# Performance work log

Measured on AMD Instinct MI355X. Metric: run time of the kernel, lower is better.

The kernel has to match this reference:

```python
import jax, jax.numpy as jnp
import numpy as np

N_NODES = 50000
N_EDGES = 1_600_000
IN_DIM = 128
HID = 32
HEADS = 4
NEG_SLOPE = 0.2


def setup_inputs() -> dict:
    key = jax.random.key(0)
    ks = jax.random.split(key, 6)
    h = jax.random.normal(ks[0], (N_NODES, IN_DIM), dtype=jnp.float32)
    src = jax.random.randint(ks[1], (N_EDGES,), 0, N_NODES, dtype=jnp.int32)
    dst = jax.random.randint(ks[2], (N_EDGES,), 0, N_NODES, dtype=jnp.int32)
    s = 1.0 / np.sqrt(IN_DIM)  # ~ Linear default init scale
    Wq = (jax.random.normal(ks[3], (HEADS, IN_DIM, HID), dtype=jnp.float32) * s)
    Wk = (jax.random.normal(ks[4], (HEADS, IN_DIM, HID), dtype=jnp.float32) * s)
    Wv = (jax.random.normal(ks[5], (HEADS, IN_DIM, HID), dtype=jnp.float32) * s)
    return {"h": h, "src": src, "dst": dst, "Wq": Wq, "Wk": Wk, "Wv": Wv}


def _gat_forward(h, src, dst, Wq, Wk, Wv):
    n = h.shape[0]
    # per-head projections: [H, N, D]
    q = jnp.einsum('ni,hio->hno', h, Wq)
    k = jnp.einsum('ni,hio->hno', h, Wk)
    v = jnp.einsum('ni,hio->hno', h, Wv)
    # edge scores: e = leaky_relu(<q_src, k_dst>)  -> [H, E]
    e = jax.nn.leaky_relu(jnp.einsum('hed,hed->he', q[:, src], k[:, dst]),
                          negative_slope=NEG_SLOPE)
    # segment softmax over incoming edges of each dst node
    seg_max = jax.vmap(lambda x: jax.ops.segment_max(x, dst, num_segments=n))(e)
    seg_max = jax.lax.stop_gradient(jnp.where(jnp.isfinite(seg_max), seg_max, 0.0))
    ex = jnp.exp(e - seg_max[:, dst])                       # [H, E]
    denom = jax.vmap(lambda x: jax.ops.segment_sum(x, dst, num_segments=n))(ex)
    alpha = ex / jnp.maximum(denom, 1e-9)[:, dst]           # [H, E]
    # weighted scatter-sum of source values into dst nodes: [H, N, D]
    msg = alpha[..., None] * v[:, src]
    out = jax.vmap(lambda m: jax.ops.segment_sum(m, dst, num_segments=n))(msg)
    # concat heads along feature dim -> [N, H*D]
    return out.transpose(1, 0, 2).reshape(n, HEADS * HID)


def reference(h, src, dst, Wq, Wk, Wv):
    return _gat_forward(h, src, dst, Wq, Wk, Wv)
```

## Files before the change

kernel.cpp:

```cpp
#include <hip/hip_runtime.h>
#include <hip/hip_fp16.h>

#define IN_DIM 128
#define HID 32
#define HEADS 4
#define OUTC (HEADS*HID)
#define NEG_SLOPE 0.2f
#define BSH 4
#define BN 16
#define BCAP 768
#define NBMAX 3200
#define NCOLS 384
#define WPB 192

typedef _Float16 f16x8 __attribute__((ext_vector_type(8)));
typedef float    f32x4 __attribute__((ext_vector_type(4)));

__device__ __forceinline__ unsigned short f2h(float f) {
    return __half_as_ushort(__float2half_rn(f));
}
__device__ __forceinline__ float2 h2f2(unsigned u) {
    __half2 h = *reinterpret_cast<__half2*>(&u);
    return __half22float2(h);
}
__device__ __forceinline__ float qdot(const uint4& qv, const float4& kd) {
    float2 a = h2f2(qv.x);
    float2 b = h2f2(qv.y);
    return a.x * kd.x + a.y * kd.y + b.x * kd.z + b.y * kd.w;
}
__device__ __forceinline__ void vacc(const uint4& qv, float e, float4& acc) {
    float2 a = h2f2(qv.z);
    float2 b = h2f2(qv.w);
    acc.x = fmaf(e, a.x, acc.x);
    acc.y = fmaf(e, a.y, acc.y);
    acc.z = fmaf(e, b.x, acc.z);
    acc.w = fmaf(e, b.y, acc.w);
}

__global__ __launch_bounds__(256) void prep_bin(
    const float* __restrict__ Wq, const float* __restrict__ Wk,
    const float* __restrict__ Wv, unsigned short* __restrict__ Wt,
    const int* __restrict__ src, const int* __restrict__ dst,
    int* __restrict__ gcount, unsigned* __restrict__ pairs,
    int ne, int nbuck)
{
    const int tid = threadIdx.x;

    if (blockIdx.x < WPB) {
        int idx = blockIdx.x * 256 + tid;
        if (idx < NCOLS * IN_DIM) {
            int c = idx >> 7, k = idx & 127;
            int sel = c >> 7;
            int cc  = c & 127;
            int head = cc >> 5, dcol = cc & 31;
            const float* W = (sel == 0) ? Wk : (sel == 1) ? Wq : Wv;
            Wt[idx] = f2h(W[(size_t)head * IN_DIM * HID + (size_t)k * HID + dcol]);
        }
        return;
    }

    __shared__ int hist[NBMAX];
    __shared__ int base[NBMAX];
    const int bblk = blockIdx.x - WPB;

    for (int i = tid; i < nbuck; i += 256) hist[i] = 0;
    __syncthreads();

    const int ne4 = ne >> 2;
    const int4* s4 = (const int4*)src;
    const int4* d4 = (const int4*)dst;

    int4 sv[4], dv[4];
    int loc[16], bk[16];
    bool val[4];
#pragma unroll
    for (int k = 0; k < 4; ++k) {
        int idx = bblk * 1024 + k * 256 + tid;
        val[k] = idx < ne4;
        if (val[k]) { sv[k] = s4[idx]; dv[k] = d4[idx]; }
        else { sv[k] = make_int4(0,0,0,0); dv[k] = make_int4(0,0,0,0); }
    }
#pragma unroll
    for (int k = 0; k < 4; ++k) {
        int dd[4] = { dv[k].x, dv[k].y, dv[k].z, dv[k].w };
#pragma unroll
        for (int j = 0; j < 4; ++j) {
            int b = dd[j] >> BSH;
            bk[k*4+j]  = b;
            loc[k*4+j] = val[k] ? atomicAdd(&hist[b], 1) : 0;
        }
    }
    __syncthreads();
    for (int i = tid; i < nbuck; i += 256)
        base[i] = hist[i] ? atomicAdd(&gcount[i], hist[i]) : 0;
    __syncthreads();
#pragma unroll
    for (int k = 0; k < 4; ++k) {
        if (!val[k]) continue;
        int ss[4] = { sv[k].x, sv[k].y, sv[k].z, sv[k].w };
        int dd[4] = { dv[k].x, dv[k].y, dv[k].z, dv[k].w };
#pragma unroll
        for (int j = 0; j < 4; ++j) {
            int b = bk[k*4+j];
            int p = base[b] + loc[k*4+j];
            if (p < BCAP)
                pairs[(size_t)b * BCAP + p] =
                    ((unsigned)ss[j] << BSH) | (unsigned)(dd[j] & (BN-1));
        }
    }
    if (bblk == 0 && tid == 0) {
        for (int e = ne4 * 4; e < ne; ++e) {
            int b = dst[e] >> BSH;
            int p = atomicAdd(&gcount[b], 1);
            if (p < BCAP)
                pairs[(size_t)b * BCAP + p] =
                    ((unsigned)src[e] << BSH) | (unsigned)(dst[e] & (BN-1));
        }
    }
}

__global__ __launch_bounds__(256) void gat_proj_mfma(
    const float* __restrict__ h, const unsigned short* __restrict__ Wt,
    unsigned short* __restrict__ Ko, unsigned short* __restrict__ QV, int n)
{
    __shared__ unsigned short hsm[32 * IN_DIM];
    const int tid  = threadIdx.x;
    const int row0 = blockIdx.x * 32;

    for (int idx = tid; idx < 32 * 64; idx += 256) {
        int r  = idx >> 6;
        int c2 = idx & 63;
        int gr = row0 + r;
        float2 hv = (gr < n) ? ((const float2*)h)[(size_t)gr * 64 + c2]
                             : make_float2(0.f, 0.f);
        int col = c2 * 2;
        int sc  = col ^ ((r & 7) << 3);
        __half2 packed = __floats2half2_rn(hv.x, hv.y);
        *(unsigned*)&hsm[r * IN_DIM + sc] = *(unsigned*)&packed;
    }
    __syncthreads();

    const int w = tid >> 6;
    const int l = tid & 63;
    const int l15 = l & 15;
    const int kg  = l >> 4;
    const _Float16* Wt16 = (const _Float16*)Wt;

    f32x4 acc[2][6];
#pragma unroll
    for (int rt = 0; rt < 2; ++rt)
#pragma unroll
        for (int ct = 0; ct < 6; ++ct) acc[rt][ct] = (f32x4){0.f, 0.f, 0.f, 0.f};

#pragma unroll
    for (int s = 0; s < 4; ++s) {
        int scol = (s * 32 + kg * 8) ^ ((l & 7) << 3);
        f16x8 a0 = *(const f16x8*)&hsm[l15 * IN_DIM + scol];
        f16x8 a1 = *(const f16x8*)&hsm[(l15 + 16) * IN_DIM + scol];
#pragma unroll
        for (int ct = 0; ct < 6; ++ct) {
            int c = w * 96 + ct * 16 + l15;
            f16x8 b = *(const f16x8*)&Wt16[(size_t)c * IN_DIM + s * 32 + kg * 8];
            acc[0][ct] = __builtin_amdgcn_mfma_f32_16x16x32_f16(a0, b, acc[0][ct], 0, 0, 0);
            acc[1][ct] = __builtin_amdgcn_mfma_f32_16x16x32_f16(a1, b, acc[1][ct], 0, 0, 0);
        }
    }

#pragma unroll
    for (int rt = 0; rt < 2; ++rt) {
#pragma unroll
        for (int ct = 0; ct < 6; ++ct) {
            int cD = w * 96 + ct * 16 + l15;
#pragma unroll
            for (int r = 0; r < 4; ++r) {
                int node = row0 + rt * 16 + kg * 4 + r;
                if (node >= n) continue;
                float v = acc[rt][ct][r];
                if (cD < 128) {
                    Ko[(size_t)node * OUTC + cD] = f2h(v);
                } else if (cD < 256) {
                    int cq = cD - 128;
                    QV[(size_t)node * 256 + (cq >> 2) * 8 + (cq & 3)] = f2h(v);
                } else {
                    int cv = cD - 256;
                    QV[(size_t)node * 256 + (cv >> 2) * 8 + (cv & 3) + 4] = f2h(v);
                }
            }
        }
    }
}

__global__ __launch_bounds__(256) void gat_bucket(
    const unsigned* __restrict__ pairs, const int* __restrict__ gcount,
    const uint4* __restrict__ QV, const ushort4* __restrict__ K2,
    float* __restrict__ out, int n, int nbuck)
{
    __shared__ unsigned short sl[BCAP];
    __shared__ int cl[BN], cur[BN], off[BN + 1];

    const int b   = blockIdx.x;
    if (b >= nbuck) return;
    const int tid = threadIdx.x;

    if (tid < BN) cl[tid] = 0;
    __syncthreads();

    int m = gcount[b]; if (m > BCAP) m = BCAP;
    const unsigned* pb = pairs + (size_t)b * BCAP;

    for (int i = tid; i < m; i += 256) atomicAdd(&cl[pb[i] & (BN - 1)], 1);
    __syncthreads();
    if (tid == 0) {
        int acc = 0;
#pragma unroll
        for (int i = 0; i < BN; ++i) { off[i] = acc; cur[i] = acc; acc += cl[i]; }
        off[BN] = acc;
    }
    __syncthreads();
    for (int i = tid; i < m; i += 256) {
        unsigned p = pb[i];
        int pos = atomicAdd(&cur[p & (BN - 1)], 1);
        sl[pos] = (unsigned short)(p >> BSH);
    }
    __syncthreads();

    const int gi  = tid >> 5;
    const int l32 = tid & 31;

#pragma unroll
    for (int q = 0; q < BN / 8; ++q) {
        int nl   = q * 8 + gi;
        int node = b * BN + nl;
        if (node >= n) continue;

        ushort4 kh = K2[(size_t)node * 32 + l32];
        float2 k01 = h2f2(*(unsigned*)&kh.x);
        float2 k23 = h2f2(*(unsigned*)&kh.z);
        const float4 kd = make_float4(k01.x, k01.y, k23.x, k23.y);

        int j        = off[nl];
        const int je = off[nl + 1];

        float4 acc = make_float4(0.f, 0.f, 0.f, 0.f);
        float  dsum = 0.f;

        for (; j + 7 < je; j += 8) {
            int s0 = sl[j],     s1 = sl[j + 1], s2 = sl[j + 2], s3 = sl[j + 3];
            int s4 = sl[j + 4], s5 = sl[j + 5], s6 = sl[j + 6], s7 = sl[j + 7];
            uint4 w0 = QV[(size_t)s0 * 32 + l32];
            uint4 w1 = QV[(size_t)s1 * 32 + l32];
            uint4 w2 = QV[(size_t)s2 * 32 + l32];
            uint4 w3 = QV[(size_t)s3 * 32 + l32];
            uint4 w4 = QV[(size_t)s4 * 32 + l32];
            uint4 w5 = QV[(size_t)s5 * 32 + l32];
            uint4 w6 = QV[(size_t)s6 * 32 + l32];
            uint4 w7 = QV[(size_t)s7 * 32 + l32];

            float p0 = qdot(w0, kd), p1 = qdot(w1, kd);
            float p2 = qdot(w2, kd), p3 = qdot(w3, kd);
            float p4 = qdot(w4, kd), p5 = qdot(w5, kd);
            float p6 = qdot(w6, kd), p7 = qdot(w7, kd);
#pragma unroll
            for (int o = 1; o < 8; o <<= 1) {
                p0 += __shfl_xor(p0, o, 8);
                p1 += __shfl_xor(p1, o, 8);
                p2 += __shfl_xor(p2, o, 8);
                p3 += __shfl_xor(p3, o, 8);
                p4 += __shfl_xor(p4, o, 8);
                p5 += __shfl_xor(p5, o, 8);
                p6 += __shfl_xor(p6, o, 8);
                p7 += __shfl_xor(p7, o, 8);
            }
            float e0 = __expf(p0 > 0.f ? p0 : NEG_SLOPE * p0);
            float e1 = __expf(p1 > 0.f ? p1 : NEG_SLOPE * p1);
            float e2 = __expf(p2 > 0.f ? p2 : NEG_SLOPE * p2);
            float e3 = __expf(p3 > 0.f ? p3 : NEG_SLOPE * p3);
            float e4 = __expf(p4 > 0.f ? p4 : NEG_SLOPE * p4);
            float e5 = __expf(p5 > 0.f ? p5 : NEG_SLOPE * p5);
            float e6 = __expf(p6 > 0.f ? p6 : NEG_SLOPE * p6);
            float e7 = __expf(p7 > 0.f ? p7 : NEG_SLOPE * p7);
            dsum += ((e0 + e1) + (e2 + e3)) + ((e4 + e5) + (e6 + e7));
            vacc(w0, e0, acc); vacc(w1, e1, acc);
            vacc(w2, e2, acc); vacc(w3, e3, acc);
            vacc(w4, e4, acc); vacc(w5, e5, acc);
            vacc(w6, e6, acc); vacc(w7, e7, acc);
        }
        for (; j + 3 < je; j += 4) {
            int s0 = sl[j], s1 = sl[j + 1], s2 = sl[j + 2], s3 = sl[j + 3];
            uint4 w0 = QV[(size_t)s0 * 32 + l32];
            uint4 w1 = QV[(size_t)s1 * 32 + l32];
            uint4 w2 = QV[(size_t)s2 * 32 + l32];
            uint4 w3 = QV[(size_t)s3 * 32 + l32];
            float p0 = qdot(w0, kd), p1 = qdot(w1, kd);
            float p2 = qdot(w2, kd), p3 = qdot(w3, kd);
#pragma unroll
            for (int o = 1; o < 8; o <<= 1) {
                p0 += __shfl_xor(p0, o, 8);
                p1 += __shfl_xor(p1, o, 8);
                p2 += __shfl_xor(p2, o, 8);
                p3 += __shfl_xor(p3, o, 8);
            }
            float e0 = __expf(p0 > 0.f ? p0 : NEG_SLOPE * p0);
            float e1 = __expf(p1 > 0.f ? p1 : NEG_SLOPE * p1);
            float e2 = __expf(p2 > 0.f ? p2 : NEG_SLOPE * p2);
            float e3 = __expf(p3 > 0.f ? p3 : NEG_SLOPE * p3);
            dsum += (e0 + e1) + (e2 + e3);
            vacc(w0, e0, acc); vacc(w1, e1, acc);
            vacc(w2, e2, acc); vacc(w3, e3, acc);
        }
        for (; j < je; ++j) {
            int s0 = sl[j];
            uint4 w0 = QV[(size_t)s0 * 32 + l32];
            float p0 = qdot(w0, kd);
#pragma unroll
            for (int o = 1; o < 8; o <<= 1) p0 += __shfl_xor(p0, o, 8);
            float e0 = __expf(p0 > 0.f ? p0 : NEG_SLOPE * p0);
            dsum += e0;
            vacc(w0, e0, acc);
        }

        float inv = 1.f / fmaxf(dsum, 1e-9f);
        float4 o; o.x = acc.x*inv; o.y = acc.y*inv; o.z = acc.z*inv; o.w = acc.w*inv;
        ((float4*)out)[(size_t)node * 32 + l32] = o;
    }
}

extern "C" void kernel_launch(void* const* d_in, const int* in_sizes, int n_in,
                              void* d_out, int out_size, void* d_ws, size_t ws_size,
                              hipStream_t stream) {
    const float* h   = (const float*)d_in[0];
    const int*   src = (const int*)d_in[1];
    const int*   dst = (const int*)d_in[2];
    const float* Wq  = (const float*)d_in[3];
    const float* Wk  = (const float*)d_in[4];
    const float* Wv  = (const float*)d_in[5];
    float* out = (float*)d_out;

    const int n     = in_sizes[0] / IN_DIM;
    const int ne    = in_sizes[1];
    const int nbuck = (n + BN - 1) >> BSH;

    unsigned short* K      = (unsigned short*)d_ws;
    unsigned short* QV     = K + (size_t)n * OUTC;
    int*            gcount = (int*)(QV + (size_t)n * 256);
    unsigned*       pairs  = (unsigned*)(gcount + NBMAX);
    unsigned short* Wt     = (unsigned short*)(pairs + (size_t)NBMAX * BCAP);

    hipMemsetAsync(gcount, 0, NBMAX * sizeof(int), stream);

    int ne4 = ne >> 2;
    int binblk = (ne4 + 1023) / 1024;
    prep_bin<<<WPB + binblk, 256, 0, stream>>>(Wq, Wk, Wv, Wt, src, dst,
                                               gcount, pairs, ne, nbuck);

    gat_proj_mfma<<<(n + 31) / 32, 256, 0, stream>>>(h, Wt, K, QV, n);

    gat_bucket<<<nbuck, 256, 0, stream>>>(pairs, gcount, (const uint4*)QV,
                                          (const ushort4*)K, out, n, nbuck);
}
```

Measured before the change: 181.8 us.

## Split Q/V layout, two-pass bucket softmax, fuse binning with projection

Zeroing of the bucket counters moves into the weight-prep kernel, which replaces the memset. Edge binning and the MFMA projection now run as one launch with block-range dispatch. Q and V are stored in separate arrays, so the bucket kernel first gathers only Q to compute exp scores into shared memory, then gathers only V in a second pass. This removes one launch and overlaps binning with projection. In exchange, the edge loop becomes two dependent gather passes over each node's edges, adds 12KB of shared memory per block that may lower occupancy, and drops the 8-way unrolled loop.

```diff
diff --git a/kernel.cpp b/kernel.cpp
--- a/kernel.cpp
+++ b/kernel.cpp
@@ -23,109 +23,111 @@
     __half2 h = *reinterpret_cast<__half2*>(&u);
     return __half22float2(h);
 }
-__device__ __forceinline__ float qdot(const uint4& qv, const float4& kd) {
-    float2 a = h2f2(qv.x);
-    float2 b = h2f2(qv.y);
+__device__ __forceinline__ float qdot2(const uint2& w, const float4& kd) {
+    float2 a = h2f2(w.x);
+    float2 b = h2f2(w.y);
     return a.x * kd.x + a.y * kd.y + b.x * kd.z + b.y * kd.w;
 }
-__device__ __forceinline__ void vacc(const uint4& qv, float e, float4& acc) {
-    float2 a = h2f2(qv.z);
-    float2 b = h2f2(qv.w);
+__device__ __forceinline__ void vacc2(const uint2& w, float e, float4& acc) {
+    float2 a = h2f2(w.x);
+    float2 b = h2f2(w.y);
     acc.x = fmaf(e, a.x, acc.x);
     acc.y = fmaf(e, a.y, acc.y);
     acc.z = fmaf(e, b.x, acc.z);
     acc.w = fmaf(e, b.y, acc.w);
 }
 
-__global__ __launch_bounds__(256) void prep_bin(
+__global__ __launch_bounds__(256) void w_prep(
     const float* __restrict__ Wq, const float* __restrict__ Wk,
     const float* __restrict__ Wv, unsigned short* __restrict__ Wt,
+    int* __restrict__ gcount)
+{
+    int idx = blockIdx.x * 256 + threadIdx.x;
+    if (idx < NBMAX) gcount[idx] = 0;
+    if (idx >= NCOLS * IN_DIM) return;
+    int c = idx >> 7, k = idx & 127;
+    int sel = c >> 7;
+    int cc  = c & 127;
+    int head = cc >> 5, dcol = cc & 31;
+    const float* W = (sel == 0) ? Wk : (sel == 1) ? Wq : Wv;
+    Wt[idx] = f2h(W[(size_t)head * IN_DIM * HID + (size_t)k * HID + dcol]);
+}
+
+__global__ __launch_bounds__(256) void bin_proj(
     const int* __restrict__ src, const int* __restrict__ dst,
     int* __restrict__ gcount, unsigned* __restrict__ pairs,
-    int ne, int nbuck)
+    const float* __restrict__ h, const unsigned short* __restrict__ Wt,
+    unsigned short* __restrict__ K, unsigned short* __restrict__ Qa,
+    unsigned short* __restrict__ Va,
+    int ne, int nbuck, int binblk, int n)
 {
+    __shared__ __align__(16) char smem_raw[2 * NBMAX * 4];
     const int tid = threadIdx.x;
 
-    if (blockIdx.x < WPB) {
-        int idx = blockIdx.x * 256 + tid;
-        if (idx < NCOLS * IN_DIM) {
-            int c = idx >> 7, k = idx & 127;
-            int sel = c >> 7;
-            int cc  = c & 127;
-            int head = cc >> 5, dcol = cc & 31;
-            const float* W = (sel == 0) ? Wk : (sel == 1) ? Wq : Wv;
-            Wt[idx] = f2h(W[(size_t)head * IN_DIM * HID + (size_t)k * HID + dcol]);
+    if ((int)blockIdx.x < binblk) {
+        int* hist = (int*)smem_raw;
+        int* base = hist + NBMAX;
+        const int bblk = blockIdx.x;
+
+        for (int i = tid; i < nbuck; i += 256) hist[i] = 0;
+        __syncthreads();
+
+        const int ne4 = ne >> 2;
+        const int4* s4 = (const int4*)src;
+        const int4* d4 = (const int4*)dst;
+
+        int4 sv[4], dv[4];
+        int loc[16], bk[16];
+        bool val[4];
+#pragma unroll
+        for (int k2 = 0; k2 < 4; ++k2) {
+            int idx = bblk * 1024 + k2 * 256 + tid;
+            val[k2] = idx < ne4;
+            if (val[k2]) { sv[k2] = s4[idx]; dv[k2] = d4[idx]; }
+            else { sv[k2] = make_int4(0,0,0,0); dv[k2] = make_int4(0,0,0,0); }
+        }
+#pragma unroll
+        for (int k2 = 0; k2 < 4; ++k2) {
+            int dd[4] = { dv[k2].x, dv[k2].y, dv[k2].z, dv[k2].w };
+#pragma unroll
+            for (int j = 0; j < 4; ++j) {
+                int b = dd[j] >> BSH;
+                bk[k2*4+j]  = b;
+                loc[k2*4+j] = val[k2] ? atomicAdd(&hist[b], 1) : 0;
+            }
+        }
+        __syncthreads();
+        for (int i = tid; i < nbuck; i += 256)
+            base[i] = hist[i] ? atomicAdd(&gcount[i], hist[i]) : 0;
+        __syncthreads();
+#pragma unroll
+        for (int k2 = 0; k2 < 4; ++k2) {
+            if (!val[k2]) continue;
+            int ss[4] = { sv[k2].x, sv[k2].y, sv[k2].z, sv[k2].w };
+            int dd[4] = { dv[k2].x, dv[k2].y, dv[k2].z, dv[k2].w };
+#pragma unroll
+            for (int j = 0; j < 4; ++j) {
+                int b = bk[k2*4+j];
+                int p = base[b] + loc[k2*4+j];
+                if (p < BCAP)
+                    pairs[(size_t)b * BCAP + p] =
+                        ((unsigned)ss[j] << BSH) | (unsigned)(dd[j] & (BN-1));
+            }
+        }
+        if (bblk == 0 && tid == 0) {
+            for (int e = ne4 * 4; e < ne; ++e) {
+                int b = dst[e] >> BSH;
+                int p = atomicAdd(&gcount[b], 1);
+                if (p < BCAP)
+                    pairs[(size_t)b * BCAP + p] =
+                        ((unsigned)src[e] << BSH) | (unsigned)(dst[e] & (BN-1));
+            }
         }
         return;
     }
 
-    __shared__ int hist[NBMAX];
-    __shared__ int base[NBMAX];
-    const int bblk = blockIdx.x - WPB;
-
-    for (int i = tid; i < nbuck; i += 256) hist[i] = 0;
-    __syncthreads();
-
-    const int ne4 = ne >> 2;
-    const int4* s4 = (const int4*)src;
-    const int4* d4 = (const int4*)dst;
-
-    int4 sv[4], dv[4];
-    int loc[16], bk[16];
-    bool val[4];
-#pragma unroll
-    for (int k = 0; k < 4; ++k) {
-        int idx = bblk * 1024 + k * 256 + tid;
-        val[k] = idx < ne4;
-        if (val[k]) { sv[k] = s4[idx]; dv[k] = d4[idx]; }
-        else { sv[k] = make_int4(0,0,0,0); dv[k] = make_int4(0,0,0,0); }
-    }
-#pragma unroll
-    for (int k = 0; k < 4; ++k) {
-        int dd[4] = { dv[k].x, dv[k].y, dv[k].z, dv[k].w };
-#pragma unroll
-        for (int j = 0; j < 4; ++j) {
-            int b = dd[j] >> BSH;
-            bk[k*4+j]  = b;
-            loc[k*4+j] = val[k] ? atomicAdd(&hist[b], 1) : 0;
-        }
-    }
-    __syncthreads();
-    for (int i = tid; i < nbuck; i += 256)
-        base[i] = hist[i] ? atomicAdd(&gcount[i], hist[i]) : 0;
-    __syncthreads();
-#pragma unroll
-    for (int k = 0; k < 4; ++k) {
-        if (!val[k]) continue;
-        int ss[4] = { sv[k].x, sv[k].y, sv[k].z, sv[k].w };
-        int dd[4] = { dv[k].x, dv[k].y, dv[k].z, dv[k].w };
-#pragma unroll
-        for (int j = 0; j < 4; ++j) {
-            int b = bk[k*4+j];
-            int p = base[b] + loc[k*4+j];
-            if (p < BCAP)
-                pairs[(size_t)b * BCAP + p] =
-                    ((unsigned)ss[j] << BSH) | (unsigned)(dd[j] & (BN-1));
-        }
-    }
-    if (bblk == 0 && tid == 0) {
-        for (int e = ne4 * 4; e < ne; ++e) {
-            int b = dst[e] >> BSH;
-            int p = atomicAdd(&gcount[b], 1);
-            if (p < BCAP)
-                pairs[(size_t)b * BCAP + p] =
-                    ((unsigned)src[e] << BSH) | (unsigned)(dst[e] & (BN-1));
-        }
-    }
-}
-
-__global__ __launch_bounds__(256) void gat_proj_mfma(
-    const float* __restrict__ h, const unsigned short* __restrict__ Wt,
-    unsigned short* __restrict__ Ko, unsigned short* __restrict__ QV, int n)
-{
-    __shared__ unsigned short hsm[32 * IN_DIM];
-    const int tid  = threadIdx.x;
-    const int row0 = blockIdx.x * 32;
+    unsigned short* hsm = (unsigned short*)smem_raw;
+    const int row0 = (blockIdx.x - binblk) * 32;
 
     for (int idx = tid; idx < 32 * 64; idx += 256) {
         int r  = idx >> 6;
@@ -175,15 +177,13 @@
             for (int r = 0; r < 4; ++r) {
                 int node = row0 + rt * 16 + kg * 4 + r;
                 if (node >= n) continue;
-                float v = acc[rt][ct][r];
+                unsigned short hv = f2h(acc[rt][ct][r]);
                 if (cD < 128) {
-                    Ko[(size_t)node * OUTC + cD] = f2h(v);
+                    K[(size_t)node * OUTC + cD] = hv;
                 } else if (cD < 256) {
-                    int cq = cD - 128;
-                    QV[(size_t)node * 256 + (cq >> 2) * 8 + (cq & 3)] = f2h(v);
+                    Qa[(size_t)node * OUTC + (cD - 128)] = hv;
                 } else {
-                    int cv = cD - 256;
-                    QV[(size_t)node * 256 + (cv >> 2) * 8 + (cv & 3) + 4] = f2h(v);
+                    Va[(size_t)node * OUTC + (cD - 256)] = hv;
                 }
             }
         }
@@ -192,13 +192,15 @@
 
 __global__ __launch_bounds__(256) void gat_bucket(
     const unsigned* __restrict__ pairs, const int* __restrict__ gcount,
-    const uint4* __restrict__ QV, const ushort4* __restrict__ K2,
+    const uint2* __restrict__ Q2, const uint2* __restrict__ V2,
+    const ushort4* __restrict__ K4,
     float* __restrict__ out, int n, int nbuck)
 {
     __shared__ unsigned short sl[BCAP];
+    __shared__ float exls[BCAP * 4];
     __shared__ int cl[BN], cur[BN], off[BN + 1];
 
-    const int b   = blockIdx.x;
+    const int b = blockIdx.x;
     if (b >= nbuck) return;
     const int tid = threadIdx.x;
 
@@ -211,10 +213,10 @@
     for (int i = tid; i < m; i += 256) atomicAdd(&cl[pb[i] & (BN - 1)], 1);
     __syncthreads();
     if (tid == 0) {
-        int acc = 0;
-#pragma unroll
-        for (int i = 0; i < BN; ++i) { off[i] = acc; cur[i] = acc; acc += cl[i]; }
-        off[BN] = acc;
+        int a = 0;
+#pragma unroll
+        for (int i = 0; i < BN; ++i) { off[i] = a; cur[i] = a; a += cl[i]; }
+        off[BN] = a;
     }
     __syncthreads();
     for (int i = tid; i < m; i += 256) {
@@ -224,8 +226,67 @@
     }
     __syncthreads();
 
-    const int gi  = tid >> 5;
-    const int l32 = tid & 31;
+    const int gi   = tid >> 5;
+    const int l32  = tid & 31;
+    const int hsel = l32 >> 3;
+    const bool wr  = (l32 & 7) == 0;
+
+    float dsum[BN / 8];
+
+#pragma unroll
+    for (int q = 0; q < BN / 8; ++q) {
+        int nl   = q * 8 + gi;
+        int node = b * BN + nl;
+        float ds = 0.f;
+        if (node < n) {
+            ushort4 kh = K4[(size_t)node * 32 + l32];
+            float2 k01 = h2f2(*(unsigned*)&kh.x);
+            float2 k23 = h2f2(*(unsigned*)&kh.z);
+            const float4 kd = make_float4(k01.x, k01.y, k23.x, k23.y);
+
+            int j        = off[nl];
+            const int je = off[nl + 1];
+            for (; j + 3 < je; j += 4) {
+                int s0 = sl[j], s1 = sl[j + 1], s2 = sl[j + 2], s3 = sl[j + 3];
+                uint2 w0 = Q2[(size_t)s0 * 32 + l32];
+                uint2 w1 = Q2[(size_t)s1 * 32 + l32];
+                uint2 w2 = Q2[(size_t)s2 * 32 + l32];
+                uint2 w3 = Q2[(size_t)s3 * 32 + l32];
+                float p0 = qdot2(w0, kd), p1 = qdot2(w1, kd);
+                float p2 = qdot2(w2, kd), p3 = qdot2(w3, kd);
+#pragma unroll
+                for (int o = 1; o < 8; o <<= 1) {
+                    p0 += __shfl_xor(p0, o, 8);
+                    p1 += __shfl_xor(p1, o, 8);
+                    p2 += __shfl_xor(p2, o, 8);
+                    p3 += __shfl_xor(p3, o, 8);
+                }
+                float e0 = __expf(p0 > 0.f ? p0 : NEG_SLOPE * p0);
+                float e1 = __expf(p1 > 0.f ? p1 : NEG_SLOPE * p1);
+                float e2 = __expf(p2 > 0.f ? p2 : NEG_SLOPE * p2);
+                float e3 = __expf(p3 > 0.f ? p3 : NEG_SLOPE * p3);
+                ds += (e0 + e1) + (e2 + e3);
+                if (wr) {
+                    exls[(j    ) * 4 + hsel] = e0;
+                    exls[(j + 1) * 4 + hsel] = e1;
+                    exls[(j + 2) * 4 + hsel] = e2;
+                    exls[(j + 3) * 4 + hsel] = e3;
+                }
+            }
+            for (; j < je; ++j) {
+                int s0 = sl[j];
+                uint2 w0 = Q2[(size_t)s0 * 32 + l32];
+                float p0 = qdot2(w0, kd);
+#pragma unroll
+                for (int o = 1; o < 8; o <<= 1) p0 += __shfl_xor(p0, o, 8);
+                float e0 = __expf(p0 > 0.f ? p0 : NEG_SLOPE * p0);
+                ds += e0;
+                if (wr) exls[j * 4 + hsel] = e0;
+            }
+        }
+        dsum[q] = ds;
+    }
+    __syncthreads();
 
 #pragma unroll
     for (int q = 0; q < BN / 8; ++q) {
@@ -233,93 +294,31 @@
         int node = b * BN + nl;
         if (node >= n) continue;
 
-        ushort4 kh = K2[(size_t)node * 32 + l32];
-        float2 k01 = h2f2(*(unsigned*)&kh.x);
-        float2 k23 = h2f2(*(unsigned*)&kh.z);
-        const float4 kd = make_float4(k01.x, k01.y, k23.x, k23.y);
-
         int j        = off[nl];
         const int je = off[nl + 1];
-
         float4 acc = make_float4(0.f, 0.f, 0.f, 0.f);
-        float  dsum = 0.f;
-
-        for (; j + 7 < je; j += 8) {
-            int s0 = sl[j],     s1 = sl[j + 1], s2 = sl[j + 2], s3 = sl[j + 3];
-            int s4 = sl[j + 4], s5 = sl[j + 5], s6 = sl[j + 6], s7 = sl[j + 7];
-            uint4 w0 = QV[(size_t)s0 * 32 + l32];
-            uint4 w1 = QV[(size_t)s1 * 32 + l32];
-            uint4 w2 = QV[(size_t)s2 * 32 + l32];
-            uint4 w3 = QV[(size_t)s3 * 32 + l32];
-            uint4 w4 = QV[(size_t)s4 * 32 + l32];
-            uint4 w5 = QV[(size_t)s5 * 32 + l32];
-            uint4 w6 = QV[(size_t)s6 * 32 + l32];
-            uint4 w7 = QV[(size_t)s7 * 32 + l32];
-
-            float p0 = qdot(w0, kd), p1 = qdot(w1, kd);
-            float p2 = qdot(w2, kd), p3 = qdot(w3, kd);
-            float p4 = qdot(w4, kd), p5 = qdot(w5, kd);
-            float p6 = qdot(w6, kd), p7 = qdot(w7, kd);
-#pragma unroll
-            for (int o = 1; o < 8; o <<= 1) {
-                p0 += __shfl_xor(p0, o, 8);
-                p1 += __shfl_xor(p1, o, 8);
-                p2 += __shfl_xor(p2, o, 8);
-                p3 += __shfl_xor(p3, o, 8);
-                p4 += __shfl_xor(p4, o, 8);
-                p5 += __shfl_xor(p5, o, 8);
-                p6 += __shfl_xor(p6, o, 8);
-                p7 += __shfl_xor(p7, o, 8);
-            }
-            float e0 = __expf(p0 > 0.f ? p0 : NEG_SLOPE * p0);
-            float e1 = __expf(p1 > 0.f ? p1 : NEG_SLOPE * p1);
-            float e2 = __expf(p2 > 0.f ? p2 : NEG_SLOPE * p2);
-            float e3 = __expf(p3 > 0.f ? p3 : NEG_SLOPE * p3);
-            float e4 = __expf(p4 > 0.f ? p4 : NEG_SLOPE * p4);
-            float e5 = __expf(p5 > 0.f ? p5 : NEG_SLOPE * p5);
-            float e6 = __expf(p6 > 0.f ? p6 : NEG_SLOPE * p6);
-            float e7 = __expf(p7 > 0.f ? p7 : NEG_SLOPE * p7);
-            dsum += ((e0 + e1) + (e2 + e3)) + ((e4 + e5) + (e6 + e7));
-            vacc(w0, e0, acc); vacc(w1, e1, acc);
-            vacc(w2, e2, acc); vacc(w3, e3, acc);
-            vacc(w4, e4, acc); vacc(w5, e5, acc);
-            vacc(w6, e6, acc); vacc(w7, e7, acc);
-        }
+
         for (; j + 3 < je; j += 4) {
             int s0 = sl[j], s1 = sl[j + 1], s2 = sl[j + 2], s3 = sl[j + 3];
-            uint4 w0 = QV[(size_t)s0 * 32 + l32];
-            uint4 w1 = QV[(size_t)s1 * 32 + l32];
-            uint4 w2 = QV[(size_t)s2 * 32 + l32];
-            uint4 w3 = QV[(size_t)s3 * 32 + l32];
-            float p0 = qdot(w0, kd), p1 = qdot(w1, kd);
-            float p2 = qdot(w2, kd), p3 = qdot(w3, kd);
-#pragma unroll
-            for (int o = 1; o < 8; o <<= 1) {
-                p0 += __shfl_xor(p0, o, 8);
-                p1 += __shfl_xor(p1, o, 8);
-                p2 += __shfl_xor(p2, o, 8);
-                p3 += __shfl_xor(p3, o, 8);
-            }
-            float e0 = __expf(p0 > 0.f ? p0 : NEG_SLOPE * p0);
-            float e1 = __expf(p1 > 0.f ? p1 : NEG_SLOPE * p1);
-            float e2 = __expf(p2 > 0.f ? p2 : NEG_SLOPE * p2);
-            float e3 = __expf(p3 > 0.f ? p3 : NEG_SLOPE * p3);
-            dsum += (e0 + e1) + (e2 + e3);
-            vacc(w0, e0, acc); vacc(w1, e1, acc);
-            vacc(w2, e2, acc); vacc(w3, e3, acc);
+            uint2 w0 = V2[(size_t)s0 * 32 + l32];
+            uint2 w1 = V2[(size_t)s1 * 32 + l32];
+            uint2 w2 = V2[(size_t)s2 * 32 + l32];
+            uint2 w3 = V2[(size_t)s3 * 32 + l32];
+            float e0 = exls[(j    ) * 4 + hsel];
+            float e1 = exls[(j + 1) * 4 + hsel];
+            float e2 = exls[(j + 2) * 4 + hsel];
+            float e3 = exls[(j + 3) * 4 + hsel];
+            vacc2(w0, e0, acc); vacc2(w1, e1, acc);
+            vacc2(w2, e2, acc); vacc2(w3, e3, acc);
         }
         for (; j < je; ++j) {
             int s0 = sl[j];
-            uint4 w0 = QV[(size_t)s0 * 32 + l32];
-            float p0 = qdot(w0, kd);
-#pragma unroll
-            for (int o = 1; o < 8; o <<= 1) p0 += __shfl_xor(p0, o, 8);
-            float e0 = __expf(p0 > 0.f ? p0 : NEG_SLOPE * p0);
-            dsum += e0;
-            vacc(w0, e0, acc);
-        }
-
-        float inv = 1.f / fmaxf(dsum, 1e-9f);
+            uint2 w0 = V2[(size_t)s0 * 32 + l32];
+            float e0 = exls[j * 4 + hsel];
+            vacc2(w0, e0, acc);
+        }
+
+        float inv = 1.f / fmaxf(dsum[q], 1e-9f);
         float4 o; o.x = acc.x*inv; o.y = acc.y*inv; o.z = acc.z*inv; o.w = acc.w*inv;
         ((float4*)out)[(size_t)node * 32 + l32] = o;
     }
@@ -341,20 +340,21 @@
     const int nbuck = (n + BN - 1) >> BSH;
 
     unsigned short* K      = (unsigned short*)d_ws;
-    unsigned short* QV     = K + (size_t)n * OUTC;
-    int*            gcount = (int*)(QV + (size_t)n * 256);
+    unsigned short* Qa     = K  + (size_t)n * OUTC;
+    unsigned short* Va     = Qa + (size_t)n * OUTC;
+    int*            gcount = (int*)(Va + (size_t)n * OUTC);
     unsigned*       pairs  = (unsigned*)(gcount + NBMAX);
     unsigned short* Wt     = (unsigned short*)(pairs + (size_t)NBMAX * BCAP);
 
-    hipMemsetAsync(gcount, 0, NBMAX * sizeof(int), stream);
-
-    int ne4 = ne >> 2;
-    int binblk = (ne4 + 1023) / 1024;
-    prep_bin<<<WPB + binblk, 256, 0, stream>>>(Wq, Wk, Wv, Wt, src, dst,
-                                               gcount, pairs, ne, nbuck);
-
-    gat_proj_mfma<<<(n + 31) / 32, 256, 0, stream>>>(h, Wt, K, QV, n);
-
-    gat_bucket<<<nbuck, 256, 0, stream>>>(pairs, gcount, (const uint4*)QV,
-                                          (const ushort4*)K, out, n, nbuck);
-}
+    w_prep<<<WPB, 256, 0, stream>>>(Wq, Wk, Wv, Wt, gcount);
+
+    int ne4     = ne >> 2;
+    int binblk  = (ne4 + 1023) / 1024;
+    int projblk = (n + 31) / 32;
+    bin_proj<<<binblk + projblk, 256, 0, stream>>>(
+        src, dst, gcount, pairs, h, Wt, K, Qa, Va, ne, nbuck, binblk, n);
+
+    gat_bucket<<<nbuck, 256, 0, stream>>>(pairs, gcount, (const uint2*)Qa,
+                                          (const uint2*)Va, (const ushort4*)K,
+                                          out, n, nbuck);
+}
```

Measured after the change: 171.6 us. 5.6% less time.
